# Kernel optimization log

Measured on AMD Instinct MI355X. Metric: run time of the kernel, lower is better.

## Reference

```python
import jax, jax.numpy as jnp
import numpy as np
from jax import lax

NUM_HEADS = 4
OUT_DIM = 384
HEAD_DIM = 96
STRIDE_Q = 2
STRIDE_KV = 2
EPS = 1e-6
SCALE = HEAD_DIM ** -0.5


def _layernorm(x, g, b):
    m = jnp.mean(x, axis=-1, keepdims=True)
    v = jnp.mean((x - m) ** 2, axis=-1, keepdims=True)
    return (x - m) * lax.rsqrt(v + EPS) * g + b


def _pool(x, w, h, wd, stride):
    # x: [B, nh, N, hd] -> depthwise conv stride-s -> [B, nh, oh*ow, hd]
    B, nh, N, hd = x.shape
    x = x.reshape(B * nh, h, wd, hd).transpose(0, 3, 1, 2)  # NCHW
    y = lax.conv_general_dilated(x, w, (stride, stride), ((1, 1), (1, 1)),
                                 feature_group_count=hd)
    oh, ow = y.shape[2], y.shape[3]
    y = y.reshape(B, nh, hd, oh * ow).transpose(0, 1, 3, 2)
    return y, (oh, ow)


def _add_rel_pos(attn, q, q_size, k_size, rel_h, rel_w):
    qh, qw = q_size
    kh, kw = k_size
    B, nh, _, hd = q.shape
    qhr = max(kh / qh, 1.0); khr = max(qh / kh, 1.0)
    dh = (jnp.arange(qh)[:, None] * qhr - jnp.arange(kh)[None, :] * khr
          + (kh - 1) * khr).astype(jnp.int32)
    qwr = max(kw / qw, 1.0); kwr = max(qw / kw, 1.0)
    dw = (jnp.arange(qw)[:, None] * qwr - jnp.arange(kw)[None, :] * kwr
          + (kw - 1) * kwr).astype(jnp.int32)
    Reh = rel_h[dh]  # [qh, kh, hd]
    Rew = rel_w[dw]  # [qw, kw, hd]
    qr = q.reshape(B, nh, qh, qw, hd)
    eh = jnp.einsum('byhwc,hkc->byhwk', qr, Reh)
    ew = jnp.einsum('byhwc,wkc->byhwk', qr, Rew)
    a = attn.reshape(B, nh, qh, qw, kh, kw) + eh[..., :, None] + ew[..., None, :]
    return a.reshape(B, nh, qh * qw, kh * kw)


def setup_inputs() -> dict:
    key = jax.random.key(0)
    ks = jax.random.split(key, 8)
    B, N, IN_DIM = 16, 3136, 192
    return {
        'hidden_states': jax.random.normal(ks[0], (B, N, IN_DIM), jnp.float32),
        'qkv_w': jax.random.normal(ks[1], (IN_DIM, 3 * OUT_DIM), jnp.float32) * 0.02,
        'qkv_b': jax.random.normal(ks[2], (3 * OUT_DIM,), jnp.float32) * 0.02,
        'pool_q_w': jax.random.normal(ks[3], (HEAD_DIM, 1, 3, 3), jnp.float32) * 0.1,
        'pool_k_w': jax.random.normal(ks[4], (HEAD_DIM, 1, 3, 3), jnp.float32) * 0.1,
        'pool_v_w': jax.random.normal(ks[5], (HEAD_DIM, 1, 3, 3), jnp.float32) * 0.1,
        'ln_q_g': jnp.ones((HEAD_DIM,), jnp.float32),
        'ln_q_b': jnp.zeros((HEAD_DIM,), jnp.float32),
        'ln_k_g': jnp.ones((HEAD_DIM,), jnp.float32),
        'ln_k_b': jnp.zeros((HEAD_DIM,), jnp.float32),
        'ln_v_g': jnp.ones((HEAD_DIM,), jnp.float32),
        'ln_v_b': jnp.zeros((HEAD_DIM,), jnp.float32),
        'rel_h': jax.random.normal(ks[6], (55, HEAD_DIM), jnp.float32) * 0.02,
        'rel_w': jax.random.normal(ks[7], (55, HEAD_DIM), jnp.float32) * 0.02,
        'height': 56,
        'width': 56,
    }


def reference(hidden_states, qkv_w, qkv_b, pool_q_w, pool_k_w, pool_v_w,
              ln_q_g, ln_q_b, ln_k_g, ln_k_b, ln_v_g, ln_v_b,
              rel_h, rel_w, height, width):
    B, N, _ = hidden_states.shape
    qkv = (hidden_states @ qkv_w + qkv_b).reshape(B, N, 3, NUM_HEADS, HEAD_DIM)
    qkv = qkv.transpose(2, 0, 3, 1, 4)  # [3, B, nh, N, hd]
    q, k, v = qkv[0], qkv[1], qkv[2]

    q, q_size = _pool(q, pool_q_w, height, width, STRIDE_Q)
    q = _layernorm(q, ln_q_g, ln_q_b)
    k, k_size = _pool(k, pool_k_w, height, width, STRIDE_KV)
    k = _layernorm(k, ln_k_g, ln_k_b)
    v, _ = _pool(v, pool_v_w, height, width, STRIDE_KV)
    v = _layernorm(v, ln_v_g, ln_v_b)

    attn = jnp.einsum('bhqd,bhkd->bhqk', q * SCALE, k)
    attn = _add_rel_pos(attn, q, q_size, k_size, rel_h, rel_w)
    attn = jax.nn.softmax(attn, axis=-1)
    out = jnp.einsum('bhqk,bhkd->bhqd', attn, v)
    out = out + q  # residual pooling (no cls token)
    out = out.transpose(0, 2, 1, 3).reshape(B, -1, OUT_DIM)
    return out
```

## Files before the change

### kernel.cpp

```cpp
#include <hip/hip_runtime.h>

#define DEVI __device__ __forceinline__

typedef __attribute__((ext_vector_type(8))) short short8;
typedef __attribute__((ext_vector_type(4))) short short4v;
typedef __attribute__((ext_vector_type(4))) float f32x4;
typedef __attribute__((ext_vector_type(4))) unsigned int u32x4;

#define ATTN_SCALE 0.10206207261596575f
#define LOG2E      1.4426950408889634f
#define KSCALE     (ATTN_SCALE * LOG2E)

DEVI unsigned short f2bf(float f){
  unsigned u = __float_as_uint(f);
  u += 0x7fff + ((u >> 16) & 1);
  return (unsigned short)(u >> 16);
}
DEVI float bf2f(unsigned short h){ return __uint_as_float(((unsigned)h) << 16); }

DEVI void gload16(const void* g, void* l){
  __builtin_amdgcn_global_load_lds((const __attribute__((address_space(1))) void*)g,
                                   (__attribute__((address_space(3))) void*)l, 16, 0, 0);
}

DEVI f32x4 mfma16(short8 a, short8 b, f32x4 c){
  return __builtin_amdgcn_mfma_f32_16x16x32_bf16(a, b, c, 0, 0, 0);
}

__global__ __launch_bounds__(256) void k_convert(const float4* __restrict__ hs4,
    const float* __restrict__ w, const float* __restrict__ rh, const float* __restrict__ rw,
    unsigned short* __restrict__ hsb, unsigned short* __restrict__ wt,
    unsigned short* __restrict__ rhb, unsigned short* __restrict__ rwb){
  const int stride = gridDim.x * 256;
  const int t0 = blockIdx.x * 256 + threadIdx.x;
  const int n4 = (50176 * 192) / 4;
  for (int i = t0; i < n4; i += stride){
    float4 v = hs4[i];
    uint2 p;
    p.x = (unsigned)f2bf(v.x) | ((unsigned)f2bf(v.y) << 16);
    p.y = (unsigned)f2bf(v.z) | ((unsigned)f2bf(v.w) << 16);
    ((uint2*)hsb)[i] = p;
  }
  for (int i = t0; i < 192 * 1152; i += stride){
    int k = i / 1152, n = i - k * 1152;
    wt[n * 192 + k] = f2bf(w[i]);
  }
  for (int i = t0; i < 55 * 96; i += stride){
    rhb[i] = f2bf(rh[i] * LOG2E);
    rwb[i] = f2bf(rw[i] * LOG2E);
  }
}

__global__ __launch_bounds__(256) void k_gemm(const unsigned short* __restrict__ A,
    const unsigned short* __restrict__ Bt,
    const float* __restrict__ bias, unsigned short* __restrict__ C){
  __shared__ unsigned short sA[2][128 * 64];
  __shared__ unsigned short sB[2][128 * 64];
  const int bid = (blockIdx.x & 7) * 441 + (blockIdx.x >> 3);
  const int bn = bid % 9, bm = bid / 9;
  const int tid = threadIdx.x, w = tid >> 6, l = tid & 63;
  const int wr = (w >> 1) * 64, wc = (w & 1) * 64;
  const int l15 = l & 15, l4 = l >> 4;
  const f32x4 z4 = {0.f, 0.f, 0.f, 0.f};
  f32x4 acc[4][4];
#pragma unroll
  for (int i = 0; i < 4; ++i)
#pragma unroll
    for (int j = 0; j < 4; ++j) acc[i][j] = z4;

  auto stage = [&](int kk, int buf){
    const int k0 = kk * 64;
#pragma unroll
    for (int i = 0; i < 4; ++i){
      const int ib = (w * 4 + i) << 10;
      const int Lb = ib + (l << 4);
      const int r  = Lb >> 7;
      const int g  = ((Lb >> 4) & 7) ^ (r & 7);
      gload16((const char*)A  + (size_t)(bm * 128 + r) * 384 + k0 * 2 + g * 16, (char*)sA[buf] + ib);
      gload16((const char*)Bt + (size_t)(bn * 128 + r) * 384 + k0 * 2 + g * 16, (char*)sB[buf] + ib);
    }
  };

  stage(0, 0);
  __syncthreads();
  for (int kk = 0; kk < 3; ++kk){
    const int buf = kk & 1;
    if (kk < 2) stage(kk + 1, buf ^ 1);
#pragma unroll
    for (int ks = 0; ks < 2; ++ks){
      short8 av[4], bv[4];
#pragma unroll
      for (int mf = 0; mf < 4; ++mf){
        const int r = wr + mf * 16 + l15;
        const int slot = (ks * 4 + l4) ^ (r & 7);
        av[mf] = *(const short8*)(sA[buf] + r * 64 + slot * 8);
      }
#pragma unroll
      for (int nf = 0; nf < 4; ++nf){
        const int r = wc + nf * 16 + l15;
        const int slot = (ks * 4 + l4) ^ (r & 7);
        bv[nf] = *(const short8*)(sB[buf] + r * 64 + slot * 8);
      }
#pragma unroll
      for (int mf = 0; mf < 4; ++mf)
#pragma unroll
        for (int nf = 0; nf < 4; ++nf)
          acc[mf][nf] = mfma16(bv[nf], av[mf], acc[mf][nf]);
    }
    if (kk < 2) __syncthreads();
  }

  __syncthreads();
  unsigned short* sC = (unsigned short*)sA;
#pragma unroll
  for (int nf = 0; nf < 4; ++nf){
    const int colq = wc + nf * 16 + l4 * 4;
    const float4 b4 = *(const float4*)(bias + bn * 128 + colq);
#pragma unroll
    for (int mf = 0; mf < 4; ++mf){
      const int row = wr + mf * 16 + l15;
      short4v p;
      p[0] = (short)f2bf(acc[mf][nf][0] + b4.x);
      p[1] = (short)f2bf(acc[mf][nf][1] + b4.y);
      p[2] = (short)f2bf(acc[mf][nf][2] + b4.z);
      p[3] = (short)f2bf(acc[mf][nf][3] + b4.w);
      const int slot = (colq >> 3) ^ (row & 7);
      *(short4v*)(sC + row * 128 + slot * 8 + (colq & 7)) = p;
    }
  }
  __syncthreads();
#pragma unroll
  for (int i = 0; i < 8; ++i){
    const int row = i * 16 + w * 4 + l4;
    const int slot = l15 ^ (row & 7);
    const short8 v = *(const short8*)(sC + row * 128 + slot * 8);
    *(short8*)(C + (size_t)(bm * 128 + row) * 1152 + bn * 128 + l15 * 8) = v;
  }
}

__global__ __launch_bounds__(384) void k_pool_ln(const unsigned short* __restrict__ qkv,
    const float* __restrict__ wq, const float* __restrict__ wk, const float* __restrict__ wv,
    const float* __restrict__ gq, const float* __restrict__ bq,
    const float* __restrict__ gk, const float* __restrict__ bk,
    const float* __restrict__ gv, const float* __restrict__ bv,
    unsigned short* __restrict__ qp, unsigned short* __restrict__ kp,
    unsigned short* __restrict__ vpt, float* __restrict__ qpf){
  __shared__ float swt[9 * 96];
  __shared__ float sg[96], sb[96];
  __shared__ float sbuf[28 * 96];
  const int bid = blockIdx.x;
  const int oy = bid % 28, h = (bid / 28) & 3, b = (bid / 112) & 15, which = bid / 1792;
  const float* wsel = which == 0 ? wq : (which == 1 ? wk : wv);
  const float* gsel = which == 0 ? gq : (which == 1 ? gk : gv);
  const float* bsel = which == 0 ? bq : (which == 1 ? bk : bv);
  const int tid = threadIdx.x;
  for (int i = tid; i < 864; i += 384){
    const int d = i / 9, t = i - d * 9;
    swt[t * 96 + d] = wsel[i];
  }
  if (tid < 96){ sg[tid] = gsel[tid]; sb[tid] = bsel[tid]; }
  __syncthreads();

  const int colbase = which * 384 + h * 96;
  if (tid < 336){
    const int ox = tid / 12, d0 = (tid - ox * 12) * 8;
    float acc[8] = {0.f,0.f,0.f,0.f,0.f,0.f,0.f,0.f};
#pragma unroll
    for (int ky = 0; ky < 3; ++ky){
      const int iy = oy * 2 + ky - 1;
      if ((unsigned)iy >= 56u) continue;
      const unsigned short* rowp = qkv + (size_t)(b * 3136 + iy * 56) * 1152 + colbase + d0;
#pragma unroll
      for (int kx = 0; kx < 3; ++kx){
        const int ix = ox * 2 + kx - 1;
        if ((unsigned)ix >= 56u) continue;
        const u32x4 raw = *(const u32x4*)(rowp + (size_t)ix * 1152);
        const float* wv8 = swt + (ky * 3 + kx) * 96 + d0;
        const float4 wa = *(const float4*)wv8;
        const float4 wb = *(const float4*)(wv8 + 4);
        acc[0] += __uint_as_float(raw[0] << 16)         * wa.x;
        acc[1] += __uint_as_float(raw[0] & 0xffff0000u) * wa.y;
        acc[2] += __uint_as_float(raw[1] << 16)         * wa.z;
        acc[3] += __uint_as_float(raw[1] & 0xffff0000u) * wa.w;
        acc[4] += __uint_as_float(raw[2] << 16)         * wb.x;
        acc[5] += __uint_as_float(raw[2] & 0xffff0000u) * wb.y;
        acc[6] += __uint_as_float(raw[3] << 16)         * wb.z;
        acc[7] += __uint_as_float(raw[3] & 0xffff0000u) * wb.w;
      }
    }
    *(float4*)(sbuf + ox * 96 + d0)     = *(float4*)acc;
    *(float4*)(sbuf + ox * 96 + d0 + 4) = *(float4*)(acc + 4);
  }
  __syncthreads();

  const int grp = tid >> 3, l8 = tid & 7;
  if (grp < 28){
    const int ox = grp, d0 = l8 * 12;
    float x[12];
    *(float4*)x       = *(const float4*)(sbuf + ox * 96 + d0);
    *(float4*)(x + 4) = *(const float4*)(sbuf + ox * 96 + d0 + 4);
    *(float4*)(x + 8) = *(const float4*)(sbuf + ox * 96 + d0 + 8);
    float s = 0.f, ss = 0.f;
#pragma unroll
    for (int j = 0; j < 12; ++j){ s += x[j]; ss += x[j] * x[j]; }
#pragma unroll
    for (int d = 1; d < 8; d <<= 1){ s += __shfl_xor(s, d); ss += __shfl_xor(ss, d); }
    const float mean = s * (1.f / 96.f);
    const float var  = ss * (1.f / 96.f) - mean * mean;
    const float rstd = rsqrtf(var + 1e-6f);
    const int n = oy * 28 + ox;
    const size_t bh = (size_t)(b * 4 + h);
    float y[12];
#pragma unroll
    for (int j = 0; j < 12; ++j)
      y[j] = (x[j] - mean) * rstd * sg[d0 + j] + sb[d0 + j];
    if (which == 0){
      const size_t idx = (bh * 784 + n) * 96 + d0;
#pragma unroll
      for (int c = 0; c < 3; ++c){
        short4v p;
        p[0] = (short)f2bf(y[c*4]);   p[1] = (short)f2bf(y[c*4+1]);
        p[2] = (short)f2bf(y[c*4+2]); p[3] = (short)f2bf(y[c*4+3]);
        *(short4v*)(qp + idx + c * 4) = p;
        *(float4*)(qpf + idx + c * 4) = *(const float4*)(y + c * 4);
      }
    } else if (which == 1){
      const size_t idx = (bh * 784 + n) * 160;
#pragma unroll
      for (int c = 0; c < 3; ++c){
        short4v p;
        p[0] = (short)f2bf(y[c*4]   * KSCALE); p[1] = (short)f2bf(y[c*4+1] * KSCALE);
        p[2] = (short)f2bf(y[c*4+2] * KSCALE); p[3] = (short)f2bf(y[c*4+3] * KSCALE);
        *(short4v*)(kp + idx + d0 + c * 4) = p;
      }
      short8 oh;
#pragma unroll
      for (int jj = 0; jj < 8; ++jj){
        const int pcol = 96 + l8 * 8 + jj;
        unsigned short v = 0;
        if (pcol == 96 + oy)  v = 0x3F80;
        if (pcol == 128 + ox) v = 0x3F80;
        oh[jj] = (short)v;
      }
      *(short8*)(kp + idx + 96 + l8 * 8) = oh;
    } else {
#pragma unroll
      for (int j = 0; j < 12; ++j)
        vpt[(bh * 96 + d0 + j) * 784 + n] = f2bf(y[j]);
    }
  }
}

__global__ __launch_bounds__(512, 4) void k_attn(
    const unsigned short* __restrict__ qp, const unsigned short* __restrict__ kp,
    const unsigned short* __restrict__ vpt, const float* __restrict__ qpf,
    const unsigned short* __restrict__ rhb, const unsigned short* __restrict__ rwb,
    float* __restrict__ out){
  __shared__ unsigned short sKm[2][64 * 128];
  __shared__ unsigned short sKe[2][64 * 32];
  __shared__ unsigned short sV[96 * 64];

  const int s = blockIdx.x, xcd = s & 7, slot = s >> 3;
  const int bh = xcd * 8 + slot / 7, qb = slot - (slot / 7) * 7;
  const int b = bh >> 2, h = bh & 3;
  const int tid = threadIdx.x, w = tid >> 6, l = tid & 63;
  const int l15 = l & 15, l4 = l >> 4;
  const size_t baseq = (size_t)bh * 784 * 96;
  const size_t basek = (size_t)bh * 784 * 160;
  const f32x4 z4 = {0.f, 0.f, 0.f, 0.f};
  const int qrl = w * 16 + l15;
  int q_l = qb * 128 + qrl; if (q_l > 783) q_l = 783;

  auto stageK = [&](int t, int buf){
    int krr = t * 64;
#pragma unroll
    for (int rd = 0; rd < 2; ++rd){
      const int off = rd * 8192 + (tid << 4);
      const int row = off >> 8;
      const int gr  = (off >> 4) & 15;
      const int sg_ = (gr & 8) | ((gr ^ row) & 7);
      int kr = krr + row; if (kr > 783) kr = 783;
      gload16((const char*)kp + ((size_t)kr * 160 + basek + sg_ * 8) * 2,
              (char*)sKm[buf] + off);
    }
    if (tid < 256){
      const int off = tid << 4;
      const int row = off >> 6;
      const int gr  = (off >> 4) & 3;
      const int sg_ = (gr ^ (row >> 1)) & 3;
      int kr = krr + row; if (kr > 783) kr = 783;
      gload16((const char*)kp + ((size_t)kr * 160 + basek + 128 + sg_ * 8) * 2,
              (char*)sKe[buf] + off);
    }
  };
  short8 vreg[2];
  auto loadV = [&](int t){
    if (tid < 384){
#pragma unroll
      for (int i = 0; i < 2; ++i){
        const int off = (tid * 2 + i) << 4;
        const int r = off >> 7;
        const int g = ((off >> 4) & 7) ^ (r & 7);
        int koff = t * 64 + g * 8; if (koff + 8 > 784) koff = 0;
        vreg[i] = *(const short8*)(vpt + (size_t)(bh * 96 + r) * 784 + koff);
      }
    }
  };
  auto writeV = [&](){
    if (tid < 384){
#pragma unroll
      for (int i = 0; i < 2; ++i)
        *(short8*)((char*)sV + ((tid * 2 + i) << 4)) = vreg[i];
    }
  };

  stageK(0, 0);
  loadV(0);

  short8 qf[5];
#pragma unroll
  for (int ks = 0; ks < 3; ++ks)
    qf[ks] = *(const short8*)(qp + baseq + (size_t)q_l * 96 + ks * 32 + l4 * 8);

  const int hh = (q_l * 2341) >> 16;
  const int ww = q_l - hh * 28;
  const int h0 = (qb * 128) / 28;

  {
    unsigned short* sGh = sKm[1];
    unsigned short* sGw = sKm[1] + 4096;
    f32x4 gh[3] = {z4, z4, z4}, gw[4] = {z4, z4, z4, z4};
#pragma unroll
    for (int nf = 0; nf < 3; ++nf){
      int j = h0 + nf * 16 + l15; if (j > 54) j = 54;
#pragma unroll
      for (int ks = 0; ks < 3; ++ks)
        gh[nf] = mfma16(*(const short8*)(rhb + j * 96 + ks * 32 + l4 * 8), qf[ks], gh[nf]);
    }
#pragma unroll
    for (int nf = 0; nf < 4; ++nf){
      int j = nf * 16 + l15; if (j > 54) j = 54;
#pragma unroll
      for (int ks = 0; ks < 3; ++ks)
        gw[nf] = mfma16(*(const short8*)(rwb + j * 96 + ks * 32 + l4 * 8), qf[ks], gw[nf]);
    }
    if (l4 == 0){
      *(short4v*)(sGh + qrl * 32 + 28) = (short4v)0;
      *(short4v*)(sGw + qrl * 32 + 28) = (short4v)0;
    }
#pragma unroll
    for (int nf = 0; nf < 3; ++nf)
#pragma unroll
      for (int reg = 0; reg < 4; ++reg){
        const int j = h0 + nf * 16 + l4 * 4 + reg;
        const int kh = hh + 27 - j;
        if ((unsigned)kh < 28u) sGh[qrl * 32 + kh] = f2bf(gh[nf][reg]);
      }
#pragma unroll
    for (int nf = 0; nf < 4; ++nf)
#pragma unroll
      for (int reg = 0; reg < 4; ++reg){
        const int j = nf * 16 + l4 * 4 + reg;
        const int kw = ww + 27 - j;
        if ((unsigned)kw < 28u) sGw[qrl * 32 + kw] = f2bf(gw[nf][reg]);
      }
    qf[3] = *(const short8*)(sGh + qrl * 32 + l4 * 8);
    qf[4] = *(const short8*)(sGw + qrl * 32 + l4 * 8);
  }

  float m = -1e30f, lsum = 0.f;
  f32x4 acc[6];
#pragma unroll
  for (int i = 0; i < 6; ++i) acc[i] = z4;

  writeV();
  __syncthreads();

  for (int kt = 0; kt < 13; ++kt){
    const int cur = kt & 1;
    if (kt < 12){ loadV(kt + 1); stageK(kt + 1, cur ^ 1); }

    f32x4 sfr[4] = {z4, z4, z4, z4};
#pragma unroll
    for (int ks = 0; ks < 4; ++ks){
      const int g = ks * 4 + l4;
#pragma unroll
      for (int nf = 0; nf < 4; ++nf){
        const int r = nf * 16 + l15;
        const int sl = (g & 8) | ((g ^ r) & 7);
        const short8 kb = *(const short8*)(sKm[cur] + r * 128 + sl * 8);
        sfr[nf] = mfma16(kb, qf[ks], sfr[nf]);
      }
    }
#pragma unroll
    for (int nf = 0; nf < 4; ++nf){
      const int r = nf * 16 + l15;
      const int sl = (l4 ^ (r >> 1)) & 3;
      const short8 kb = *(const short8*)(sKe[cur] + r * 32 + sl * 8);
      sfr[nf] = mfma16(kb, qf[4], sfr[nf]);
    }
    if (kt == 12){
      const f32x4 m30 = {-1e30f, -1e30f, -1e30f, -1e30f};
      sfr[1] = m30; sfr[2] = m30; sfr[3] = m30;
    }

    float mx;
    {
      float a0 = fmaxf(fmaxf(sfr[0][0], sfr[0][1]), fmaxf(sfr[0][2], sfr[0][3]));
      float a1 = fmaxf(fmaxf(sfr[1][0], sfr[1][1]), fmaxf(sfr[1][2], sfr[1][3]));
      float a2 = fmaxf(fmaxf(sfr[2][0], sfr[2][1]), fmaxf(sfr[2][2], sfr[2][3]));
      float a3 = fmaxf(fmaxf(sfr[3][0], sfr[3][1]), fmaxf(sfr[3][2], sfr[3][3]));
      mx = fmaxf(fmaxf(a0, a1), fmaxf(a2, a3));
    }
    mx = fmaxf(mx, __shfl_xor(mx, 16));
    mx = fmaxf(mx, __shfl_xor(mx, 32));
    const float mn = fmaxf(m, mx);
    const float al = exp2f(m - mn);
    m = mn;
    float sum;
    {
#pragma unroll
      for (int nf = 0; nf < 4; ++nf)
#pragma unroll
        for (int reg = 0; reg < 4; ++reg)
          sfr[nf][reg] = exp2f(sfr[nf][reg] - mn);
      float s0 = (sfr[0][0] + sfr[0][1]) + (sfr[0][2] + sfr[0][3]);
      float s1 = (sfr[1][0] + sfr[1][1]) + (sfr[1][2] + sfr[1][3]);
      float s2 = (sfr[2][0] + sfr[2][1]) + (sfr[2][2] + sfr[2][3]);
      float s3 = (sfr[3][0] + sfr[3][1]) + (sfr[3][2] + sfr[3][3]);
      sum = (s0 + s1) + (s2 + s3);
    }
    sum += __shfl_xor(sum, 16);
    sum += __shfl_xor(sum, 32);
    lsum = lsum * al + sum;

    __syncthreads();

    unsigned short* sPp = sKm[cur];
#pragma unroll
    for (int nf = 0; nf < 4; ++nf){
      short4v p4;
      p4[0] = (short)f2bf(sfr[nf][0]); p4[1] = (short)f2bf(sfr[nf][1]);
      p4[2] = (short)f2bf(sfr[nf][2]); p4[3] = (short)f2bf(sfr[nf][3]);
      char* dst = (char*)sPp + qrl * 128 + (((nf * 2 + (l4 >> 1)) ^ (l15 & 7)) << 4) + ((l4 & 1) << 3);
      *(short4v*)dst = p4;
    }
#pragma unroll
    for (int i = 0; i < 6; ++i)
#pragma unroll
      for (int reg = 0; reg < 4; ++reg)
        acc[i][reg] *= al;

#pragma unroll
    for (int ks = 0; ks < 2; ++ks){
      const short8 pb = *(const short8*)((char*)sPp + qrl * 128 + (((ks * 4 + l4) ^ (l15 & 7)) << 4));
#pragma unroll
      for (int nf = 0; nf < 6; ++nf){
        const int r = nf * 16 + l15;
        const int sl = (ks * 4 + l4) ^ (r & 7);
        const short8 vb = *(const short8*)(sV + r * 64 + sl * 8);
        acc[nf] = mfma16(vb, pb, acc[nf]);
      }
    }

    if (kt < 12){
      __syncthreads();
      writeV();
      __syncthreads();
    }
  }

  const int qg = qb * 128 + qrl;
  if (qg < 784){
    const float rcp = 1.f / lsum;
    const float* qrow = qpf + baseq + (size_t)qg * 96;
    float* orow = out + ((size_t)b * 784 + qg) * 384 + h * 96;
#pragma unroll
    for (int nf = 0; nf < 6; ++nf)
#pragma unroll
      for (int reg = 0; reg < 4; ++reg){
        const int d = nf * 16 + l4 * 4 + reg;
        orow[d] = acc[nf][reg] * rcp + qrow[d];
      }
  }
}

extern "C" void kernel_launch(void* const* d_in, const int* in_sizes, int n_in,
                              void* d_out, int out_size, void* d_ws, size_t ws_size,
                              hipStream_t stream){
  const float* hs  = (const float*)d_in[0];
  const float* qw  = (const float*)d_in[1];
  const float* qb  = (const float*)d_in[2];
  const float* pwq = (const float*)d_in[3];
  const float* pwk = (const float*)d_in[4];
  const float* pwv = (const float*)d_in[5];
  const float* gq  = (const float*)d_in[6];
  const float* bq  = (const float*)d_in[7];
  const float* gk  = (const float*)d_in[8];
  const float* bk  = (const float*)d_in[9];
  const float* gv  = (const float*)d_in[10];
  const float* bv  = (const float*)d_in[11];
  const float* rh  = (const float*)d_in[12];
  const float* rw  = (const float*)d_in[13];
  float* out = (float*)d_out;

  char* ws = (char*)d_ws;
  size_t off = 0;
  auto take = [&](size_t n)->char*{ char* p = ws + off; off += (n + 255) & ~(size_t)255; return p; };
  unsigned short* hsb = (unsigned short*)take((size_t)50176 * 192 * 2);
  unsigned short* wtb = (unsigned short*)take((size_t)1152 * 192 * 2);
  unsigned short* qkv = (unsigned short*)take((size_t)50176 * 1152 * 2);
  unsigned short* qpb = (unsigned short*)take((size_t)64 * 784 * 96 * 2);
  unsigned short* kpb = (unsigned short*)take((size_t)64 * 784 * 160 * 2);
  unsigned short* vpt = (unsigned short*)take((size_t)64 * 784 * 96 * 2);
  float* qpf          = (float*)take((size_t)64 * 784 * 96 * 4);
  unsigned short* rhb = (unsigned short*)take((size_t)55 * 96 * 2);
  unsigned short* rwb = (unsigned short*)take((size_t)55 * 96 * 2);

  hipLaunchKernelGGL(k_convert, dim3(1024), dim3(256), 0, stream,
                     (const float4*)hs, qw, rh, rw, hsb, wtb, rhb, rwb);
  hipLaunchKernelGGL(k_gemm, dim3(392 * 9), dim3(256), 0, stream, hsb, wtb, qb, qkv);
  hipLaunchKernelGGL(k_pool_ln, dim3(5376), dim3(384), 0, stream, qkv,
                     pwq, pwk, pwv, gq, bq, gk, bk, gv, bv, qpb, kpb, vpt, qpf);
  hipLaunchKernelGGL(k_attn, dim3(448), dim3(512), 0, stream,
                     qpb, kpb, vpt, qpf, rhb, rwb, out);
}
```

Measured before the change: 259.6 us.

## Double-buffer V via direct global-to-LDS loads, drop fp32 Q copy, add setprio

V tiles now go straight from global memory into a double-buffered LDS array using global_load_lds, replacing the register staging and write-back. P gets its own LDS buffer, which removes two of the three barriers per key tile. The fp32 copy of pooled Q is dropped, and the residual add reads the bf16 Q instead, cutting a 19 MB write and read. s_setprio is wrapped around the MFMA sections. The trade-offs are a small loss of residual precision and more LDS per block, which may reduce occupancy.

```diff
diff --git a/kernel.cpp b/kernel.cpp
--- a/kernel.cpp
+++ b/kernel.cpp
@@ -144,7 +144,7 @@
     const float* __restrict__ gk, const float* __restrict__ bk,
     const float* __restrict__ gv, const float* __restrict__ bv,
     unsigned short* __restrict__ qp, unsigned short* __restrict__ kp,
-    unsigned short* __restrict__ vpt, float* __restrict__ qpf){
+    unsigned short* __restrict__ vpt){
   __shared__ float swt[9 * 96];
   __shared__ float sg[96], sb[96];
   __shared__ float sbuf[28 * 96];
@@ -222,7 +222,6 @@
         p[0] = (short)f2bf(y[c*4]);   p[1] = (short)f2bf(y[c*4+1]);
         p[2] = (short)f2bf(y[c*4+2]); p[3] = (short)f2bf(y[c*4+3]);
         *(short4v*)(qp + idx + c * 4) = p;
-        *(float4*)(qpf + idx + c * 4) = *(const float4*)(y + c * 4);
       }
     } else if (which == 1){
       const size_t idx = (bh * 784 + n) * 160;
@@ -253,12 +252,13 @@
 
 __global__ __launch_bounds__(512, 4) void k_attn(
     const unsigned short* __restrict__ qp, const unsigned short* __restrict__ kp,
-    const unsigned short* __restrict__ vpt, const float* __restrict__ qpf,
+    const unsigned short* __restrict__ vpt,
     const unsigned short* __restrict__ rhb, const unsigned short* __restrict__ rwb,
     float* __restrict__ out){
   __shared__ unsigned short sKm[2][64 * 128];
   __shared__ unsigned short sKe[2][64 * 32];
-  __shared__ unsigned short sV[96 * 64];
+  __shared__ unsigned short sV[2][96 * 64];
+  __shared__ unsigned short sP[128 * 64];
 
   const int s = blockIdx.x, xcd = s & 7, slot = s >> 3;
   const int bh = xcd * 8 + slot / 7, qb = slot - (slot / 7) * 7;
@@ -293,29 +293,22 @@
               (char*)sKe[buf] + off);
     }
   };
-  short8 vreg[2];
-  auto loadV = [&](int t){
-    if (tid < 384){
+  auto stageV = [&](int t, int buf){
+    if (w < 6){
 #pragma unroll
       for (int i = 0; i < 2; ++i){
-        const int off = (tid * 2 + i) << 4;
+        const int off = w * 2048 + i * 1024 + (l << 4);
         const int r = off >> 7;
         const int g = ((off >> 4) & 7) ^ (r & 7);
         int koff = t * 64 + g * 8; if (koff + 8 > 784) koff = 0;
-        vreg[i] = *(const short8*)(vpt + (size_t)(bh * 96 + r) * 784 + koff);
+        gload16((const char*)vpt + ((size_t)(bh * 96 + r) * 784 + koff) * 2,
+                (char*)sV[buf] + off);
       }
     }
   };
-  auto writeV = [&](){
-    if (tid < 384){
-#pragma unroll
-      for (int i = 0; i < 2; ++i)
-        *(short8*)((char*)sV + ((tid * 2 + i) << 4)) = vreg[i];
-    }
-  };
 
   stageK(0, 0);
-  loadV(0);
+  stageV(0, 0);
 
   short8 qf[5];
 #pragma unroll
@@ -373,14 +366,14 @@
 #pragma unroll
   for (int i = 0; i < 6; ++i) acc[i] = z4;
 
-  writeV();
   __syncthreads();
 
   for (int kt = 0; kt < 13; ++kt){
     const int cur = kt & 1;
-    if (kt < 12){ loadV(kt + 1); stageK(kt + 1, cur ^ 1); }
+    if (kt < 12){ stageV(kt + 1, cur ^ 1); stageK(kt + 1, cur ^ 1); }
 
     f32x4 sfr[4] = {z4, z4, z4, z4};
+    __builtin_amdgcn_s_setprio(1);
 #pragma unroll
     for (int ks = 0; ks < 4; ++ks){
       const int g = ks * 4 + l4;
@@ -399,6 +392,7 @@
       const short8 kb = *(const short8*)(sKe[cur] + r * 32 + sl * 8);
       sfr[nf] = mfma16(kb, qf[4], sfr[nf]);
     }
+    __builtin_amdgcn_s_setprio(0);
     if (kt == 12){
       const f32x4 m30 = {-1e30f, -1e30f, -1e30f, -1e30f};
       sfr[1] = m30; sfr[2] = m30; sfr[3] = m30;
@@ -434,15 +428,12 @@
     sum += __shfl_xor(sum, 32);
     lsum = lsum * al + sum;
 
-    __syncthreads();
-
-    unsigned short* sPp = sKm[cur];
 #pragma unroll
     for (int nf = 0; nf < 4; ++nf){
       short4v p4;
       p4[0] = (short)f2bf(sfr[nf][0]); p4[1] = (short)f2bf(sfr[nf][1]);
       p4[2] = (short)f2bf(sfr[nf][2]); p4[3] = (short)f2bf(sfr[nf][3]);
-      char* dst = (char*)sPp + qrl * 128 + (((nf * 2 + (l4 >> 1)) ^ (l15 & 7)) << 4) + ((l4 & 1) << 3);
+      char* dst = (char*)sP + qrl * 128 + (((nf * 2 + (l4 >> 1)) ^ (l15 & 7)) << 4) + ((l4 & 1) << 3);
       *(short4v*)dst = p4;
     }
 #pragma unroll
@@ -451,37 +442,36 @@
       for (int reg = 0; reg < 4; ++reg)
         acc[i][reg] *= al;
 
+    __builtin_amdgcn_s_setprio(1);
 #pragma unroll
     for (int ks = 0; ks < 2; ++ks){
-      const short8 pb = *(const short8*)((char*)sPp + qrl * 128 + (((ks * 4 + l4) ^ (l15 & 7)) << 4));
+      const short8 pb = *(const short8*)((char*)sP + qrl * 128 + (((ks * 4 + l4) ^ (l15 & 7)) << 4));
 #pragma unroll
       for (int nf = 0; nf < 6; ++nf){
         const int r = nf * 16 + l15;
         const int sl = (ks * 4 + l4) ^ (r & 7);
-        const short8 vb = *(const short8*)(sV + r * 64 + sl * 8);
+        const short8 vb = *(const short8*)(sV[cur] + r * 64 + sl * 8);
         acc[nf] = mfma16(vb, pb, acc[nf]);
       }
     }
-
-    if (kt < 12){
-      __syncthreads();
-      writeV();
-      __syncthreads();
-    }
+    __builtin_amdgcn_s_setprio(0);
+
+    if (kt < 12) __syncthreads();
   }
 
   const int qg = qb * 128 + qrl;
   if (qg < 784){
     const float rcp = 1.f / lsum;
-    const float* qrow = qpf + baseq + (size_t)qg * 96;
+    const unsigned short* qrow = qp + baseq + (size_t)qg * 96;
     float* orow = out + ((size_t)b * 784 + qg) * 384 + h * 96;
 #pragma unroll
-    for (int nf = 0; nf < 6; ++nf)
-#pragma unroll
-      for (int reg = 0; reg < 4; ++reg){
-        const int d = nf * 16 + l4 * 4 + reg;
-        orow[d] = acc[nf][reg] * rcp + qrow[d];
-      }
+    for (int nf = 0; nf < 6; ++nf){
+      const int d0 = nf * 16 + l4 * 4;
+      const short4v q4 = *(const short4v*)(qrow + d0);
+#pragma unroll
+      for (int reg = 0; reg < 4; ++reg)
+        orow[d0 + reg] = acc[nf][reg] * rcp + bf2f((unsigned short)q4[reg]);
+    }
   }
 }
 
@@ -513,7 +503,6 @@
   unsigned short* qpb = (unsigned short*)take((size_t)64 * 784 * 96 * 2);
   unsigned short* kpb = (unsigned short*)take((size_t)64 * 784 * 160 * 2);
   unsigned short* vpt = (unsigned short*)take((size_t)64 * 784 * 96 * 2);
-  float* qpf          = (float*)take((size_t)64 * 784 * 96 * 4);
   unsigned short* rhb = (unsigned short*)take((size_t)55 * 96 * 2);
   unsigned short* rwb = (unsigned short*)take((size_t)55 * 96 * 2);
 
@@ -521,7 +510,7 @@
                      (const float4*)hs, qw, rh, rw, hsb, wtb, rhb, rwb);
   hipLaunchKernelGGL(k_gemm, dim3(392 * 9), dim3(256), 0, stream, hsb, wtb, qb, qkv);
   hipLaunchKernelGGL(k_pool_ln, dim3(5376), dim3(384), 0, stream, qkv,
-                     pwq, pwk, pwv, gq, bq, gk, bk, gv, bv, qpb, kpb, vpt, qpf);
+                     pwq, pwk, pwv, gq, bq, gk, bk, gv, bv, qpb, kpb, vpt);
   hipLaunchKernelGGL(k_attn, dim3(448), dim3(512), 0, stream,
-                     qpb, kpb, vpt, qpf, rhb, rwb, out);
-}
+                     qpb, kpb, vpt, rhb, rwb, out);
+}
```

Result: faster. 245.0 us (-5.6%).
